# Performance work log

Hardware: AMD Instinct MI355X
Metric: run time of the kernel (lower is better)

## Reference

```python
import jax, jax.numpy as jnp
import numpy as np

BATCH = 16384
IN_DIM = 256
UNITS = 256


def setup_inputs() -> dict:
    key = jax.random.key(0)
    ks = jax.random.split(key, 5)
    scale = 1.0 / np.sqrt(IN_DIM + UNITS)
    return {
        "x": jax.random.normal(ks[0], (BATCH, IN_DIM), dtype=jnp.float32),
        "prev_h": jax.random.normal(ks[1], (BATCH, UNITS), dtype=jnp.float32),
        "Wz": jax.random.normal(ks[2], (IN_DIM + UNITS, UNITS), dtype=jnp.float32) * scale,
        "bz": jnp.zeros((UNITS,), dtype=jnp.float32),
        "Wr": jax.random.normal(ks[3], (IN_DIM + UNITS, UNITS), dtype=jnp.float32) * scale,
        "br": jnp.zeros((UNITS,), dtype=jnp.float32),
        "Ws": jax.random.normal(ks[4], (IN_DIM + UNITS, UNITS), dtype=jnp.float32) * scale,
        "bs": jnp.zeros((UNITS,), dtype=jnp.float32),
    }


def reference(x, prev_h, Wz, bz, Wr, br, Ws, bs):
    # concat order matches the TF module: [prev_h, x]
    concat = jnp.concatenate([prev_h, x], axis=1)  # [B, units+in_dim]
    z = jax.nn.sigmoid(concat @ Wz + bz)
    r = jax.nn.sigmoid(concat @ Wr + br)
    concat_cand = jnp.concatenate([r * prev_h, x], axis=1)
    h_tilda = jnp.tanh(concat_cand @ Ws + bs)
    h_new = (1.0 - z) * prev_h + z * h_tilda
    return h_new
```

## Files before the change

kernel.cpp:

```cpp
#include <hip/hip_runtime.h>
#include <hip/hip_bf16.h>


#define BATCH 16384
#define UNITS 256
#define KDIM 512
#define ROWS 32

typedef float f32x4 __attribute__((ext_vector_type(4)));
typedef __bf16 bf16x8 __attribute__((ext_vector_type(8)));
typedef unsigned short us8 __attribute__((ext_vector_type(8)));
typedef unsigned short us4v __attribute__((ext_vector_type(4)));

static __device__ __forceinline__ unsigned short f2bf(float f) {
    union { float f; unsigned u; } v; v.f = f;
    unsigned r = v.u + 0x7fffu + ((v.u >> 16) & 1u);
    return (unsigned short)(r >> 16);
}
static __device__ __forceinline__ float bf2f(unsigned short u) {
    union { unsigned u; float f; } v; v.u = ((unsigned)u) << 16;
    return v.f;
}

__global__ void pack_weights(const float* __restrict__ Wz,
                             const float* __restrict__ Wr,
                             const float* __restrict__ Ws,
                             unsigned short* __restrict__ out) {
    int gid = blockIdx.x * blockDim.x + threadIdx.x;
    int w   = gid >> 17;
    int rem = gid & 131071;
    int k = rem >> 8;
    int n = rem & 255;
    const float* W = (w == 0) ? Wz : (w == 1) ? Wr : Ws;
    float f = W[rem];
    int kt = k >> 5, kr = k & 31;
    int hi = kr >> 3, j = kr & 7;
    int nt = n >> 4,  lo = n & 15;
    int l  = hi * 16 + lo;
    out[(size_t)w * 131072 + (size_t)(((kt * 16 + nt) * 64 + l) * 8 + j)] = f2bf(f);
}

__launch_bounds__(512, 4)
__global__ void gru_main(const float* __restrict__ x,
                         const float* __restrict__ ph,
                         const float* __restrict__ bz,
                         const float* __restrict__ br,
                         const float* __restrict__ bs,
                         const unsigned short* __restrict__ Wp,
                         float* __restrict__ out) {
    __shared__ unsigned short sm[ROWS * 512];

    const int tid  = threadIdx.x;
    const int lane = tid & 63;
    const int wid  = tid >> 6;
    const int brow = blockIdx.x * ROWS;

    for (int i = tid; i < 2048; i += 512) {
        int row = i >> 6;
        int c4  = (i & 63) << 2;
        int swr = (row & 7) << 3;
        float4 a = *(const float4*)&ph[(size_t)(brow + row) * 256 + c4];
        us4v u; u.x = f2bf(a.x); u.y = f2bf(a.y); u.z = f2bf(a.z); u.w = f2bf(a.w);
        *(us4v*)&sm[row * 512 + (c4 ^ swr)] = u;
        float4 b = *(const float4*)&x[(size_t)(brow + row) * 256 + c4];
        us4v v; v.x = f2bf(b.x); v.y = f2bf(b.y); v.z = f2bf(b.z); v.w = f2bf(b.w);
        *(us4v*)&sm[row * 512 + ((256 + c4) ^ swr)] = v;
    }
    __syncthreads();

    const unsigned short* Wz_p = Wp;
    const unsigned short* Wr_p = Wp + 131072;
    const unsigned short* Ws_p = Wp + 262144;

    const int l15 = lane & 15;
    const int kg  = (lane >> 4) << 3;

    f32x4 accz[2][2] = {};
    f32x4 accr[2][2] = {};
    for (int kt = 0; kt < 16; ++kt) {
        int ak = kt * 32 + kg;
        bf16x8 a[2];
#pragma unroll
        for (int m = 0; m < 2; ++m) {
            int arow = m * 16 + l15;
            a[m] = __builtin_bit_cast(bf16x8,
                *(const us8*)&sm[arow * 512 + (ak ^ ((arow & 7) << 3))]);
        }
#pragma unroll
        for (int t = 0; t < 2; ++t) {
            int nt = wid * 2 + t;
            size_t bidx = (size_t)(((kt * 16 + nt) * 64 + lane) * 8);
            bf16x8 b0 = __builtin_bit_cast(bf16x8, *(const us8*)(Wz_p + bidx));
            bf16x8 b1 = __builtin_bit_cast(bf16x8, *(const us8*)(Wr_p + bidx));
#pragma unroll
            for (int m = 0; m < 2; ++m) {
                accz[m][t] = __builtin_amdgcn_mfma_f32_16x16x32_bf16(a[m], b0, accz[m][t], 0, 0, 0);
                accr[m][t] = __builtin_amdgcn_mfma_f32_16x16x32_bf16(a[m], b1, accr[m][t], 0, 0, 0);
            }
        }
    }
    __syncthreads();

    float pst[2][2][4];
    const int rrow0 = (lane >> 4) * 4;
#pragma unroll
    for (int t = 0; t < 2; ++t) {
        int col = wid * 32 + t * 16 + l15;
        float bzc = bz[col], brc = br[col];
#pragma unroll
        for (int m = 0; m < 2; ++m) {
#pragma unroll
            for (int i = 0; i < 4; ++i) {
                int lrow = m * 16 + rrow0 + i;
                int addr = lrow * 512 + (col ^ ((lrow & 7) << 3));
                float p = bf2f(sm[addr]);
                float z = 1.f / (1.f + __expf(-(accz[m][t][i] + bzc)));
                float r = 1.f / (1.f + __expf(-(accr[m][t][i] + brc)));
                accz[m][t][i] = z;
                pst[m][t][i]  = p;
                sm[addr] = f2bf(r * p);
            }
        }
    }
    __syncthreads();

    f32x4 accs[2][2] = {};
    for (int kt = 0; kt < 16; ++kt) {
        int ak = kt * 32 + kg;
        bf16x8 a[2];
#pragma unroll
        for (int m = 0; m < 2; ++m) {
            int arow = m * 16 + l15;
            a[m] = __builtin_bit_cast(bf16x8,
                *(const us8*)&sm[arow * 512 + (ak ^ ((arow & 7) << 3))]);
        }
#pragma unroll
        for (int t = 0; t < 2; ++t) {
            int nt = wid * 2 + t;
            size_t bidx = (size_t)(((kt * 16 + nt) * 64 + lane) * 8);
            bf16x8 b = __builtin_bit_cast(bf16x8, *(const us8*)(Ws_p + bidx));
#pragma unroll
            for (int m = 0; m < 2; ++m) {
                accs[m][t] = __builtin_amdgcn_mfma_f32_16x16x32_bf16(a[m], b, accs[m][t], 0, 0, 0);
            }
        }
    }

#pragma unroll
    for (int t = 0; t < 2; ++t) {
        int col = wid * 32 + t * 16 + l15;
        float bsc = bs[col];
#pragma unroll
        for (int m = 0; m < 2; ++m) {
#pragma unroll
            for (int i = 0; i < 4; ++i) {
                float s = accs[m][t][i] + bsc;
                float e = __expf(-2.f * fabsf(s));
                float th = (1.f - e) / (1.f + e);
                th = (s < 0.f) ? -th : th;
                float z = accz[m][t][i];
                float p = pst[m][t][i];
                int grow = brow + m * 16 + rrow0 + i;
                out[(size_t)grow * 256 + col] = (1.f - z) * p + z * th;
            }
        }
    }
}

extern "C" void kernel_launch(void* const* d_in, const int* in_sizes, int n_in,
                              void* d_out, int out_size, void* d_ws, size_t ws_size,
                              hipStream_t stream) {
    const float* x  = (const float*)d_in[0];
    const float* ph = (const float*)d_in[1];
    const float* Wz = (const float*)d_in[2];
    const float* bz = (const float*)d_in[3];
    const float* Wr = (const float*)d_in[4];
    const float* br = (const float*)d_in[5];
    const float* Ws = (const float*)d_in[6];
    const float* bs = (const float*)d_in[7];
    unsigned short* Wp = (unsigned short*)d_ws;

    hipLaunchKernelGGL(pack_weights, dim3(1536), dim3(256), 0, stream, Wz, Wr, Ws, Wp);
    hipLaunchKernelGGL(gru_main, dim3(512), dim3(512), 0, stream,
                       x, ph, bz, br, bs, Wp, (float*)d_out);
}
```

Measured before the change: 39.26 us.

## Use 64-row blocks with 16 waves, each owning one 16-column tile

Doubles the rows per block to 64 and the threads per block to 1024, so each of the 16 waves owns one 16-column tile across all 64 rows instead of two tiles over 32 rows. Each weight fragment loaded from global memory now feeds four MFMAs instead of two, which halves total weight traffic across the grid. The cost is fewer blocks (256, roughly one per CU), doubled LDS per block, and 1024-thread blocks that may lower occupancy and leave less latency hiding.

```diff
diff --git a/kernel.cpp b/kernel.cpp
--- a/kernel.cpp
+++ b/kernel.cpp
@@ -5,7 +5,7 @@
 #define BATCH 16384
 #define UNITS 256
 #define KDIM 512
-#define ROWS 32
+#define ROWS 64
 
 typedef float f32x4 __attribute__((ext_vector_type(4)));
 typedef __bf16 bf16x8 __attribute__((ext_vector_type(8)));
@@ -40,7 +40,7 @@
     out[(size_t)w * 131072 + (size_t)(((kt * 16 + nt) * 64 + l) * 8 + j)] = f2bf(f);
 }
 
-__launch_bounds__(512, 4)
+__launch_bounds__(1024, 4)
 __global__ void gru_main(const float* __restrict__ x,
                          const float* __restrict__ ph,
                          const float* __restrict__ bz,
@@ -55,7 +55,7 @@
     const int wid  = tid >> 6;
     const int brow = blockIdx.x * ROWS;
 
-    for (int i = tid; i < 2048; i += 512) {
+    for (int i = tid; i < 4096; i += 1024) {
         int row = i >> 6;
         int c4  = (i & 63) << 2;
         int swr = (row & 7) << 3;
@@ -75,91 +75,72 @@
     const int l15 = lane & 15;
     const int kg  = (lane >> 4) << 3;
 
-    f32x4 accz[2][2] = {};
-    f32x4 accr[2][2] = {};
+    f32x4 accz[4] = {};
+    f32x4 accr[4] = {};
     for (int kt = 0; kt < 16; ++kt) {
         int ak = kt * 32 + kg;
-        bf16x8 a[2];
+        size_t bidx = (size_t)(((kt * 16 + wid) * 64 + lane) * 8);
+        bf16x8 b0 = __builtin_bit_cast(bf16x8, *(const us8*)(Wz_p + bidx));
+        bf16x8 b1 = __builtin_bit_cast(bf16x8, *(const us8*)(Wr_p + bidx));
 #pragma unroll
-        for (int m = 0; m < 2; ++m) {
+        for (int m = 0; m < 4; ++m) {
             int arow = m * 16 + l15;
-            a[m] = __builtin_bit_cast(bf16x8,
+            bf16x8 a = __builtin_bit_cast(bf16x8,
                 *(const us8*)&sm[arow * 512 + (ak ^ ((arow & 7) << 3))]);
-        }
-#pragma unroll
-        for (int t = 0; t < 2; ++t) {
-            int nt = wid * 2 + t;
-            size_t bidx = (size_t)(((kt * 16 + nt) * 64 + lane) * 8);
-            bf16x8 b0 = __builtin_bit_cast(bf16x8, *(const us8*)(Wz_p + bidx));
-            bf16x8 b1 = __builtin_bit_cast(bf16x8, *(const us8*)(Wr_p + bidx));
-#pragma unroll
-            for (int m = 0; m < 2; ++m) {
-                accz[m][t] = __builtin_amdgcn_mfma_f32_16x16x32_bf16(a[m], b0, accz[m][t], 0, 0, 0);
-                accr[m][t] = __builtin_amdgcn_mfma_f32_16x16x32_bf16(a[m], b1, accr[m][t], 0, 0, 0);
-            }
+            accz[m] = __builtin_amdgcn_mfma_f32_16x16x32_bf16(a, b0, accz[m], 0, 0, 0);
+            accr[m] = __builtin_amdgcn_mfma_f32_16x16x32_bf16(a, b1, accr[m], 0, 0, 0);
         }
     }
     __syncthreads();
 
-    float pst[2][2][4];
+    float pst[4][4];
     const int rrow0 = (lane >> 4) * 4;
-#pragma unroll
-    for (int t = 0; t < 2; ++t) {
-        int col = wid * 32 + t * 16 + l15;
+    const int col   = wid * 16 + l15;
+    {
         float bzc = bz[col], brc = br[col];
 #pragma unroll
-        for (int m = 0; m < 2; ++m) {
+        for (int m = 0; m < 4; ++m) {
 #pragma unroll
             for (int i = 0; i < 4; ++i) {
                 int lrow = m * 16 + rrow0 + i;
                 int addr = lrow * 512 + (col ^ ((lrow & 7) << 3));
                 float p = bf2f(sm[addr]);
-                float z = 1.f / (1.f + __expf(-(accz[m][t][i] + bzc)));
-                float r = 1.f / (1.f + __expf(-(accr[m][t][i] + brc)));
-                accz[m][t][i] = z;
-                pst[m][t][i]  = p;
+                float z = 1.f / (1.f + __expf(-(accz[m][i] + bzc)));
+                float r = 1.f / (1.f + __expf(-(accr[m][i] + brc)));
+                accz[m][i] = z;
+                pst[m][i]  = p;
                 sm[addr] = f2bf(r * p);
             }
         }
     }
     __syncthreads();
 
-    f32x4 accs[2][2] = {};
+    f32x4 accs[4] = {};
     for (int kt = 0; kt < 16; ++kt) {
         int ak = kt * 32 + kg;
-        bf16x8 a[2];
+        size_t bidx = (size_t)(((kt * 16 + wid) * 64 + lane) * 8);
+        bf16x8 b = __builtin_bit_cast(bf16x8, *(const us8*)(Ws_p + bidx));
 #pragma unroll
-        for (int m = 0; m < 2; ++m) {
+        for (int m = 0; m < 4; ++m) {
             int arow = m * 16 + l15;
-            a[m] = __builtin_bit_cast(bf16x8,
+            bf16x8 a = __builtin_bit_cast(bf16x8,
                 *(const us8*)&sm[arow * 512 + (ak ^ ((arow & 7) << 3))]);
-        }
-#pragma unroll
-        for (int t = 0; t < 2; ++t) {
-            int nt = wid * 2 + t;
-            size_t bidx = (size_t)(((kt * 16 + nt) * 64 + lane) * 8);
-            bf16x8 b = __builtin_bit_cast(bf16x8, *(const us8*)(Ws_p + bidx));
-#pragma unroll
-            for (int m = 0; m < 2; ++m) {
-                accs[m][t] = __builtin_amdgcn_mfma_f32_16x16x32_bf16(a[m], b, accs[m][t], 0, 0, 0);
-            }
+            accs[m] = __builtin_amdgcn_mfma_f32_16x16x32_bf16(a, b, accs[m], 0, 0, 0);
         }
     }
 
-#pragma unroll
-    for (int t = 0; t < 2; ++t) {
-        int col = wid * 32 + t * 16 + l15;
+    {
         float bsc = bs[col];
 #pragma unroll
-        for (int m = 0; m < 2; ++m) {
+        for (int m = 0; m < 4; ++m) {
 #pragma unroll
             for (int i = 0; i < 4; ++i) {
-                float s = accs[m][t][i] + bsc;
+                float s = accs[m][i] + bsc;
                 float e = __expf(-2.f * fabsf(s));
                 float th = (1.f - e) / (1.f + e);
                 th = (s < 0.f) ? -th : th;
-                float z = accz[m][t][i];
-                float p = pst[m][t][i];
+                float z = accz[m][i];
+                float p = pst[m][i];
                 int grow = brow + m * 16 + rrow0 + i;
                 out[(size_t)grow * 256 + col] = (1.f - z) * p + z * th;
             }
@@ -181,6 +162,6 @@
     unsigned short* Wp = (unsigned short*)d_ws;
 
     hipLaunchKernelGGL(pack_weights, dim3(1536), dim3(256), 0, stream, Wz, Wr, Ws, Wp);
-    hipLaunchKernelGGL(gru_main, dim3(512), dim3(512), 0, stream,
+    hipLaunchKernelGGL(gru_main, dim3(256), dim3(1024), 0, stream,
                        x, ph, bz, br, bs, Wp, (float*)d_out);
 }
```

New measurement: 37.23 us. 1.05x faster.

## Load activations directly from global, prefetch weights, overlap x-part of candidate GEMM

Applied to the files above, without the earlier changes.

The main kernel no longer stages x and prev_h in shared memory. Each wave loads its A fragments directly from global memory and converts them to bf16 in registers, while the weight fragments are register-prefetched one k-step ahead. The x-portion of the candidate GEMM is now computed before the barrier, so it overlaps the gate epilogue, and only r*h goes through a smaller LDS buffer. The pack kernel is vectorised to write 8 bf16 per thread. The cost is that each wave re-reads activations from global/L2 redundantly (8 waves per block), and register pressure rises.

```diff
diff --git a/kernel.cpp b/kernel.cpp
--- a/kernel.cpp
+++ b/kernel.cpp
@@ -2,24 +2,26 @@
 #include <hip/hip_bf16.h>
 
 
-#define BATCH 16384
-#define UNITS 256
-#define KDIM 512
 #define ROWS 32
 
 typedef float f32x4 __attribute__((ext_vector_type(4)));
 typedef __bf16 bf16x8 __attribute__((ext_vector_type(8)));
 typedef unsigned short us8 __attribute__((ext_vector_type(8)));
-typedef unsigned short us4v __attribute__((ext_vector_type(4)));
 
 static __device__ __forceinline__ unsigned short f2bf(float f) {
-    union { float f; unsigned u; } v; v.f = f;
-    unsigned r = v.u + 0x7fffu + ((v.u >> 16) & 1u);
-    return (unsigned short)(r >> 16);
-}
-static __device__ __forceinline__ float bf2f(unsigned short u) {
-    union { unsigned u; float f; } v; v.u = ((unsigned)u) << 16;
-    return v.f;
+    __bf16 h = (__bf16)f;
+    return __builtin_bit_cast(unsigned short, h);
+}
+
+static __device__ __forceinline__ bf16x8 ldA(const float* __restrict__ base,
+                                             int row, int kk) {
+    const float* p = base + (size_t)row * 256 + kk;
+    float4 a = *(const float4*)p;
+    float4 b = *(const float4*)(p + 4);
+    us8 o;
+    o[0] = f2bf(a.x); o[1] = f2bf(a.y); o[2] = f2bf(a.z); o[3] = f2bf(a.w);
+    o[4] = f2bf(b.x); o[5] = f2bf(b.y); o[6] = f2bf(b.z); o[7] = f2bf(b.w);
+    return __builtin_bit_cast(bf16x8, o);
 }
 
 __global__ void pack_weights(const float* __restrict__ Wz,
@@ -27,17 +29,19 @@
                              const float* __restrict__ Ws,
                              unsigned short* __restrict__ out) {
     int gid = blockIdx.x * blockDim.x + threadIdx.x;
-    int w   = gid >> 17;
-    int rem = gid & 131071;
-    int k = rem >> 8;
-    int n = rem & 255;
+    int w    = gid >> 14;
+    int rem  = gid & 16383;
+    int kt   = rem >> 10;
+    int rem2 = rem & 1023;
+    int nt   = rem2 >> 6;
+    int lane = rem2 & 63;
+    int hi = lane >> 4, lo = lane & 15;
     const float* W = (w == 0) ? Wz : (w == 1) ? Wr : Ws;
-    float f = W[rem];
-    int kt = k >> 5, kr = k & 31;
-    int hi = kr >> 3, j = kr & 7;
-    int nt = n >> 4,  lo = n & 15;
-    int l  = hi * 16 + lo;
-    out[(size_t)w * 131072 + (size_t)(((kt * 16 + nt) * 64 + l) * 8 + j)] = f2bf(f);
+    const float* src = W + (size_t)(kt * 32 + hi * 8) * 256 + nt * 16 + lo;
+    us8 o;
+#pragma unroll
+    for (int j = 0; j < 8; ++j) o[j] = f2bf(src[(size_t)j * 256]);
+    *(us8*)&out[(size_t)w * 131072 + (size_t)(((kt * 16 + nt) * 64 + lane) * 8)] = o;
 }
 
 __launch_bounds__(512, 4)
@@ -48,123 +52,151 @@
                          const float* __restrict__ bs,
                          const unsigned short* __restrict__ Wp,
                          float* __restrict__ out) {
-    __shared__ unsigned short sm[ROWS * 512];
+    __shared__ unsigned short rhb[ROWS * 256];
 
     const int tid  = threadIdx.x;
     const int lane = tid & 63;
     const int wid  = tid >> 6;
     const int brow = blockIdx.x * ROWS;
 
-    for (int i = tid; i < 2048; i += 512) {
-        int row = i >> 6;
-        int c4  = (i & 63) << 2;
-        int swr = (row & 7) << 3;
-        float4 a = *(const float4*)&ph[(size_t)(brow + row) * 256 + c4];
-        us4v u; u.x = f2bf(a.x); u.y = f2bf(a.y); u.z = f2bf(a.z); u.w = f2bf(a.w);
-        *(us4v*)&sm[row * 512 + (c4 ^ swr)] = u;
-        float4 b = *(const float4*)&x[(size_t)(brow + row) * 256 + c4];
-        us4v v; v.x = f2bf(b.x); v.y = f2bf(b.y); v.z = f2bf(b.z); v.w = f2bf(b.w);
-        *(us4v*)&sm[row * 512 + ((256 + c4) ^ swr)] = v;
-    }
-    __syncthreads();
-
-    const unsigned short* Wz_p = Wp;
-    const unsigned short* Wr_p = Wp + 131072;
-    const unsigned short* Ws_p = Wp + 262144;
-
-    const int l15 = lane & 15;
-    const int kg  = (lane >> 4) << 3;
+    const int l15   = lane & 15;
+    const int hi    = lane >> 4;
+    const int kg    = hi << 3;
+    const int rrow0 = hi * 4;
+    const int c0    = wid * 32 + l15;
+    const int c1    = c0 + 16;
+
+    const unsigned short* WzB = Wp          + (size_t)(wid * 128 + lane) * 8;
+    const unsigned short* WrB = WzB + 131072;
+    const unsigned short* WsB = WzB + 262144;
+
+    us8 z0n = *(const us8*)WzB;        us8 z1n = *(const us8*)(WzB + 512);
+    us8 r0n = *(const us8*)WrB;        us8 r1n = *(const us8*)(WrB + 512);
+
+    const float bz0 = bz[c0], bz1 = bz[c1];
+    const float br0 = br[c0], br1 = br[c1];
+    const float bs0 = bs[c0], bs1 = bs[c1];
+
+    float pst[2][2][4];
+#pragma unroll
+    for (int m = 0; m < 2; ++m)
+#pragma unroll
+        for (int t = 0; t < 2; ++t)
+#pragma unroll
+            for (int i = 0; i < 4; ++i)
+                pst[m][t][i] = ph[(size_t)(brow + m * 16 + rrow0 + i) * 256
+                                  + (t ? c1 : c0)];
 
     f32x4 accz[2][2] = {};
     f32x4 accr[2][2] = {};
-    for (int kt = 0; kt < 16; ++kt) {
-        int ak = kt * 32 + kg;
-        bf16x8 a[2];
-#pragma unroll
-        for (int m = 0; m < 2; ++m) {
-            int arow = m * 16 + l15;
-            a[m] = __builtin_bit_cast(bf16x8,
-                *(const us8*)&sm[arow * 512 + (ak ^ ((arow & 7) << 3))]);
-        }
-#pragma unroll
-        for (int t = 0; t < 2; ++t) {
-            int nt = wid * 2 + t;
-            size_t bidx = (size_t)(((kt * 16 + nt) * 64 + lane) * 8);
-            bf16x8 b0 = __builtin_bit_cast(bf16x8, *(const us8*)(Wz_p + bidx));
-            bf16x8 b1 = __builtin_bit_cast(bf16x8, *(const us8*)(Wr_p + bidx));
-#pragma unroll
-            for (int m = 0; m < 2; ++m) {
-                accz[m][t] = __builtin_amdgcn_mfma_f32_16x16x32_bf16(a[m], b0, accz[m][t], 0, 0, 0);
-                accr[m][t] = __builtin_amdgcn_mfma_f32_16x16x32_bf16(a[m], b1, accr[m][t], 0, 0, 0);
-            }
-        }
-    }
-    __syncthreads();
-
-    float pst[2][2][4];
-    const int rrow0 = (lane >> 4) * 4;
-#pragma unroll
-    for (int t = 0; t < 2; ++t) {
-        int col = wid * 32 + t * 16 + l15;
-        float bzc = bz[col], brc = br[col];
-#pragma unroll
-        for (int m = 0; m < 2; ++m) {
+#pragma unroll
+    for (int kt = 0; kt < 8; ++kt) {
+        bf16x8 z0 = __builtin_bit_cast(bf16x8, z0n), z1 = __builtin_bit_cast(bf16x8, z1n);
+        bf16x8 r0 = __builtin_bit_cast(bf16x8, r0n), r1 = __builtin_bit_cast(bf16x8, r1n);
+        size_t no = (size_t)(kt + 1) * 8192;
+        z0n = *(const us8*)(WzB + no); z1n = *(const us8*)(WzB + no + 512);
+        r0n = *(const us8*)(WrB + no); r1n = *(const us8*)(WrB + no + 512);
+        int kk = kt * 32 + kg;
+#pragma unroll
+        for (int m = 0; m < 2; ++m) {
+            bf16x8 a = ldA(ph, brow + m * 16 + l15, kk);
+            accz[m][0] = __builtin_amdgcn_mfma_f32_16x16x32_bf16(a, z0, accz[m][0], 0, 0, 0);
+            accz[m][1] = __builtin_amdgcn_mfma_f32_16x16x32_bf16(a, z1, accz[m][1], 0, 0, 0);
+            accr[m][0] = __builtin_amdgcn_mfma_f32_16x16x32_bf16(a, r0, accr[m][0], 0, 0, 0);
+            accr[m][1] = __builtin_amdgcn_mfma_f32_16x16x32_bf16(a, r1, accr[m][1], 0, 0, 0);
+        }
+    }
+#pragma unroll
+    for (int kt = 8; kt < 16; ++kt) {
+        bf16x8 z0 = __builtin_bit_cast(bf16x8, z0n), z1 = __builtin_bit_cast(bf16x8, z1n);
+        bf16x8 r0 = __builtin_bit_cast(bf16x8, r0n), r1 = __builtin_bit_cast(bf16x8, r1n);
+        if (kt < 15) {
+            size_t no = (size_t)(kt + 1) * 8192;
+            z0n = *(const us8*)(WzB + no); z1n = *(const us8*)(WzB + no + 512);
+            r0n = *(const us8*)(WrB + no); r1n = *(const us8*)(WrB + no + 512);
+        }
+        int kk = (kt - 8) * 32 + kg;
+#pragma unroll
+        for (int m = 0; m < 2; ++m) {
+            bf16x8 a = ldA(x, brow + m * 16 + l15, kk);
+            accz[m][0] = __builtin_amdgcn_mfma_f32_16x16x32_bf16(a, z0, accz[m][0], 0, 0, 0);
+            accz[m][1] = __builtin_amdgcn_mfma_f32_16x16x32_bf16(a, z1, accz[m][1], 0, 0, 0);
+            accr[m][0] = __builtin_amdgcn_mfma_f32_16x16x32_bf16(a, r0, accr[m][0], 0, 0, 0);
+            accr[m][1] = __builtin_amdgcn_mfma_f32_16x16x32_bf16(a, r1, accr[m][1], 0, 0, 0);
+        }
+    }
+
+    us8 s0n = *(const us8*)(WsB + (size_t)8 * 8192);
+    us8 s1n = *(const us8*)(WsB + (size_t)8 * 8192 + 512);
+
+#pragma unroll
+    for (int m = 0; m < 2; ++m)
+#pragma unroll
+        for (int t = 0; t < 2; ++t)
 #pragma unroll
             for (int i = 0; i < 4; ++i) {
                 int lrow = m * 16 + rrow0 + i;
-                int addr = lrow * 512 + (col ^ ((lrow & 7) << 3));
-                float p = bf2f(sm[addr]);
-                float z = 1.f / (1.f + __expf(-(accz[m][t][i] + bzc)));
-                float r = 1.f / (1.f + __expf(-(accr[m][t][i] + brc)));
+                float z = 1.f / (1.f + __expf(-(accz[m][t][i] + (t ? bz1 : bz0))));
+                float r = 1.f / (1.f + __expf(-(accr[m][t][i] + (t ? br1 : br0))));
                 accz[m][t][i] = z;
-                pst[m][t][i]  = p;
-                sm[addr] = f2bf(r * p);
+                rhb[lrow * 256 + ((t ? c1 : c0) ^ ((lrow & 7) << 3))]
+                    = f2bf(r * pst[m][t][i]);
             }
-        }
-    }
+
+    f32x4 accs[2][2] = {};
+#pragma unroll
+    for (int kt = 8; kt < 16; ++kt) {
+        bf16x8 s0 = __builtin_bit_cast(bf16x8, s0n), s1 = __builtin_bit_cast(bf16x8, s1n);
+        if (kt < 15) {
+            size_t no = (size_t)(kt + 1) * 8192;
+            s0n = *(const us8*)(WsB + no); s1n = *(const us8*)(WsB + no + 512);
+        }
+        int kk = (kt - 8) * 32 + kg;
+#pragma unroll
+        for (int m = 0; m < 2; ++m) {
+            bf16x8 a = ldA(x, brow + m * 16 + l15, kk);
+            accs[m][0] = __builtin_amdgcn_mfma_f32_16x16x32_bf16(a, s0, accs[m][0], 0, 0, 0);
+            accs[m][1] = __builtin_amdgcn_mfma_f32_16x16x32_bf16(a, s1, accs[m][1], 0, 0, 0);
+        }
+    }
+
+    s0n = *(const us8*)WsB;
+    s1n = *(const us8*)(WsB + 512);
     __syncthreads();
 
-    f32x4 accs[2][2] = {};
-    for (int kt = 0; kt < 16; ++kt) {
+#pragma unroll
+    for (int kt = 0; kt < 8; ++kt) {
+        bf16x8 s0 = __builtin_bit_cast(bf16x8, s0n), s1 = __builtin_bit_cast(bf16x8, s1n);
+        if (kt < 7) {
+            size_t no = (size_t)(kt + 1) * 8192;
+            s0n = *(const us8*)(WsB + no); s1n = *(const us8*)(WsB + no + 512);
+        }
         int ak = kt * 32 + kg;
-        bf16x8 a[2];
 #pragma unroll
         for (int m = 0; m < 2; ++m) {
             int arow = m * 16 + l15;
-            a[m] = __builtin_bit_cast(bf16x8,
-                *(const us8*)&sm[arow * 512 + (ak ^ ((arow & 7) << 3))]);
-        }
-#pragma unroll
-        for (int t = 0; t < 2; ++t) {
-            int nt = wid * 2 + t;
-            size_t bidx = (size_t)(((kt * 16 + nt) * 64 + lane) * 8);
-            bf16x8 b = __builtin_bit_cast(bf16x8, *(const us8*)(Ws_p + bidx));
-#pragma unroll
-            for (int m = 0; m < 2; ++m) {
-                accs[m][t] = __builtin_amdgcn_mfma_f32_16x16x32_bf16(a[m], b, accs[m][t], 0, 0, 0);
-            }
-        }
-    }
-
-#pragma unroll
-    for (int t = 0; t < 2; ++t) {
-        int col = wid * 32 + t * 16 + l15;
-        float bsc = bs[col];
-#pragma unroll
-        for (int m = 0; m < 2; ++m) {
+            bf16x8 a = __builtin_bit_cast(bf16x8,
+                *(const us8*)&rhb[arow * 256 + (ak ^ ((arow & 7) << 3))]);
+            accs[m][0] = __builtin_amdgcn_mfma_f32_16x16x32_bf16(a, s0, accs[m][0], 0, 0, 0);
+            accs[m][1] = __builtin_amdgcn_mfma_f32_16x16x32_bf16(a, s1, accs[m][1], 0, 0, 0);
+        }
+    }
+
+#pragma unroll
+    for (int m = 0; m < 2; ++m)
+#pragma unroll
+        for (int t = 0; t < 2; ++t)
 #pragma unroll
             for (int i = 0; i < 4; ++i) {
-                float s = accs[m][t][i] + bsc;
+                float s = accs[m][t][i] + (t ? bs1 : bs0);
                 float e = __expf(-2.f * fabsf(s));
                 float th = (1.f - e) / (1.f + e);
                 th = (s < 0.f) ? -th : th;
                 float z = accz[m][t][i];
                 float p = pst[m][t][i];
-                int grow = brow + m * 16 + rrow0 + i;
-                out[(size_t)grow * 256 + col] = (1.f - z) * p + z * th;
+                out[(size_t)(brow + m * 16 + rrow0 + i) * 256 + (t ? c1 : c0)]
+                    = (1.f - z) * p + z * th;
             }
-        }
-    }
 }
 
 extern "C" void kernel_launch(void* const* d_in, const int* in_sizes, int n_in,
@@ -180,7 +212,7 @@
     const float* bs = (const float*)d_in[7];
     unsigned short* Wp = (unsigned short*)d_ws;
 
-    hipLaunchKernelGGL(pack_weights, dim3(1536), dim3(256), 0, stream, Wz, Wr, Ws, Wp);
+    hipLaunchKernelGGL(pack_weights, dim3(192), dim3(256), 0, stream, Wz, Wr, Ws, Wp);
     hipLaunchKernelGGL(gru_main, dim3(512), dim3(512), 0, stream,
                        x, ph, bz, br, bs, Wp, (float*)d_out);
 }
```

Result: slower. 107.9 us (+175.0%).
